# Performance work log

Measured on AMD Instinct MI355X. Metric: run time of the kernel, lower is better.

## Reference

```python
import jax, jax.numpy as jnp
import numpy as np

B, T, E, DK, H = 8, 2048, 1024, 64, 16  # dk*num_heads == embedding_dim


def setup_inputs() -> dict:
    key = jax.random.key(0)
    kx, kq, kk, kv, kl = jax.random.split(key, 5)
    x = jax.random.normal(kx, (B, T, E), dtype=jnp.float32)
    # zero-pad a random tail of each sequence so the data-derived padding mask
    # in the forward (length = count of nonzero energy[b,0,:]) is exercised
    lengths = jax.random.randint(kl, (B,), T // 2, T + 1)
    valid = (jnp.arange(T)[None, :, None] < lengths[:, None, None]).astype(jnp.float32)
    x = x * valid
    scale = 0.02
    Wq = jax.random.normal(kq, (E, DK * H), dtype=jnp.float32) * scale
    Wk = jax.random.normal(kk, (E, DK * H), dtype=jnp.float32) * scale
    Wv = jax.random.normal(kv, (E, DK * H), dtype=jnp.float32) * scale
    return {"x": x, "Wq": Wq, "Wk": Wk, "Wv": Wv}


def reference(x, Wq, Wk, Wv):
    # Q,K,V: [B, T, DK*H] (heads are fused, matching the source's bmm math)
    Q = jnp.einsum('bte,ed->btd', x, Wq)
    K = jnp.einsum('bte,ed->btd', x, Wk)
    V = jnp.einsum('bte,ed->btd', x, Wv)
    energy = jnp.einsum('btd,bsd->bts', Q, K)  # [B, T, T]
    # vectorized version of the per-batch loop: length from nonzeros of row 0,
    # then mask all key columns >= length with -inf
    lengths = jnp.sum(energy[:, 0, :] != 0, axis=-1)              # [B]
    col_mask = jnp.arange(T)[None, :] >= lengths[:, None]          # [B, T]
    energy = jnp.where(col_mask[:, None, :], -jnp.inf, energy)
    score = jax.nn.softmax(energy / jnp.sqrt(jnp.float32(DK)), axis=-1)
    return jnp.einsum('bts,bsd->btd', score, V)  # [B, T, DK*H]
```

## Files before the change

kernel.cpp:

```cpp
#include <hip/hip_runtime.h>
#include <hip/hip_bf16.h>


typedef unsigned short u16;
typedef __bf16 bf16x8 __attribute__((ext_vector_type(8)));
typedef float f32x4 __attribute__((ext_vector_type(4)));
typedef unsigned short us8 __attribute__((ext_vector_type(8)));

__device__ __forceinline__ u16 f2bf(float f) {
    union { float f; unsigned u; } x; x.f = f;
    unsigned r = x.u + 0x7FFFu + ((x.u >> 16) & 1u);
    return (u16)(r >> 16);
}
__device__ __forceinline__ u16 f2h(float f) {
    union { _Float16 h; u16 u; } c; c.h = (_Float16)f;
    return c.u;
}
__device__ __forceinline__ float h2f(u16 b) {
    union { u16 u; _Float16 h; } c; c.u = b;
    return (float)c.h;
}

__device__ __forceinline__ void gload_lds16(const void* g, void* l) {
    __builtin_amdgcn_global_load_lds(
        (const __attribute__((address_space(1))) unsigned*)g,
        (__attribute__((address_space(3))) unsigned*)l, 16, 0, 0);
}

__device__ __forceinline__ unsigned lds_off(const void* p) {
    return (unsigned)(size_t)(const __attribute__((address_space(3))) char*)p;
}
__device__ __forceinline__ bf16x8 ds_read16(unsigned a) {
    bf16x8 r;
    asm volatile("ds_read_b128 %0, %1" : "=v"(r) : "v"(a));
    return r;
}

__global__ void cast_x(const float* __restrict__ x, u16* __restrict__ o) {
    int i = blockIdx.x * 256 + threadIdx.x;
    float4 v = ((const float4*)x)[i];
    ushort4 u;
    u.x = f2bf(v.x); u.y = f2bf(v.y); u.z = f2bf(v.z); u.w = f2bf(v.w);
    ((ushort4*)o)[i] = u;
}

__global__ void transpose_cast_w(const float* __restrict__ Wq,
                                 const float* __restrict__ Wk,
                                 const float* __restrict__ Wv,
                                 u16* __restrict__ WT) {
    __shared__ float tile[32][33];
    const float* W = (blockIdx.z == 0) ? Wq : (blockIdx.z == 1) ? Wk : Wv;
    u16* T = WT + (size_t)blockIdx.z * 1048576;
    int n0 = blockIdx.x * 32, e0 = blockIdx.y * 32;
    int tx = threadIdx.x, ty = threadIdx.y;
#pragma unroll
    for (int j = 0; j < 4; ++j) {
        int e = ty + j * 8;
        tile[e][tx] = W[(size_t)(e0 + e) * 1024 + (n0 + tx)];
    }
    __syncthreads();
#pragma unroll
    for (int j = 0; j < 4; ++j) {
        int n = ty + j * 8;
        T[(size_t)(n0 + n) * 1024 + (e0 + tx)] = f2bf(tile[tx][n]);
    }
}

__global__ void calc_lengths(const float* __restrict__ x, int* __restrict__ len) {
    int b = blockIdx.x, tid = threadIdx.x;
    int cnt = 0;
    for (int t = tid; t < 2048; t += 256) {
        float4 v = *(const float4*)(x + ((size_t)b * 2048 + t) * 1024);
        cnt += (v.x != 0.f || v.y != 0.f || v.z != 0.f || v.w != 0.f) ? 1 : 0;
    }
#pragma unroll
    for (int off = 32; off; off >>= 1) cnt += __shfl_xor(cnt, off);
    __shared__ int red[4];
    int wid = tid >> 6, lane = tid & 63;
    if (!lane) red[wid] = cnt;
    __syncthreads();
    if (tid == 0) len[b] = red[0] + red[1] + red[2] + red[3];
}


#define SBAR0 __builtin_amdgcn_sched_barrier(0)

#define STAGE_T(KT, BUF) do { \
  _Pragma("unroll") for (int j_ = 0; j_ < 4; ++j_) \
      gload_lds16(A + offA[j_] + (size_t)(KT) * 64, &As[BUF][ldsC[j_]]); \
  _Pragma("unroll") for (int j_ = 0; j_ < 4; ++j_) \
      gload_lds16(B + offB[j_] + (size_t)(KT) * 64, &Bs[BUF][ldsC[j_]]); \
} while (0)

#define LD_A(S) do { \
  _Pragma("unroll") for (int mt_ = 0; mt_ < 4; ++mt_) \
    af[S][mt_] = ds_read16(rowA[mt_] + ((S) ? ps1 : ps0)); \
} while (0)
#define LD_B(S) do { \
  _Pragma("unroll") for (int nt_ = 0; nt_ < 4; ++nt_) \
    bf[S][nt_] = ds_read16(rowB[nt_] + ((S) ? ps1 : ps0)); \
} while (0)

#define MFMA_S(S) do { \
  _Pragma("unroll") for (int mt_ = 0; mt_ < 4; ++mt_) \
  _Pragma("unroll") for (int nt_ = 0; nt_ < 4; ++nt_) \
    acc[mt_][nt_] = __builtin_amdgcn_mfma_f32_16x16x32_bf16( \
        af[S][mt_], bf[S][nt_], acc[mt_][nt_], 0, 0, 0); \
} while (0)

template <int MODE>
__global__ __launch_bounds__(256, 2)
void gemm_bt(const u16* __restrict__ A, int lda, size_t sA,
             const u16* __restrict__ B, int ldb, size_t sB,
             void* __restrict__ Cv, void* __restrict__ Cv2,
             int ldc, size_t sC, int Kdim, const int* __restrict__ lenp) {
    __shared__ u16 As[2][128 * 64];
    __shared__ u16 Bs[2][128 * 64];
    const int tid = threadIdx.x;
    const int bz  = blockIdx.z;
    A += (size_t)bz * sA;
    B += (size_t)bz * sB;

    size_t bm, bn;
    if (MODE == 3) {
        int c    = blockIdx.x & 7;
        int s    = blockIdx.x >> 3;
        int half = (s >= 192) ? 1 : 0;
        int s2   = s - half * 192;
        int bx   = ((c + (half << 3)) << 3) + (s2 & 7);
        bm = (size_t)bx * 128;
        bn = (size_t)(s2 >> 3) * 128;
    } else {
        bm = (size_t)blockIdx.x * 128;
        bn = (size_t)blockIdx.y * 128;
    }

    bool skip = false;
    int kEnd = Kdim;
    if (MODE == 3) {
        int lenz = lenp[bm >> 11];
        skip = ((int)(bm & 2047) >= lenz);
    } else if (MODE == 4) {
        int lenz = lenp[bz];
        if ((int)bn >= lenz) return;
        skip = ((int)bm >= lenz);
    } else if (MODE == 5) {
        int lenz = lenp[bz];
        int r64 = (lenz + 63) & ~63;
        kEnd = r64 < Kdim ? r64 : Kdim;
    }

    const int wid = tid >> 6, lane = tid & 63;
    const int wm = wid >> 1, wn = wid & 1;
    const int q = lane >> 4, r = lane & 15;

    size_t offA[4], offB[4]; int ldsC[4];
#pragma unroll
    for (int j = 0; j < 4; ++j) {
        int c = j * 256 + tid;
        int row = c >> 3;
        int c16 = (c & 7) ^ (row & 7);
        offA[j] = (size_t)(bm + row) * lda + c16 * 8;
        offB[j] = (size_t)(bn + row) * ldb + c16 * 8;
        ldsC[j] = c * 8;
    }

    unsigned rowA[4], rowB[4], swz0, swz1;
    {
        unsigned asB = lds_off(&As[0][0]), bsB = lds_off(&Bs[0][0]);
        swz0 = (unsigned)((q ^ (r & 7)) * 16);
        swz1 = (unsigned)(((q + 4) ^ (r & 7)) * 16);
#pragma unroll
        for (int mt = 0; mt < 4; ++mt)
            rowA[mt] = asB + (unsigned)((wm * 64 + mt * 16 + r) * 128);
#pragma unroll
        for (int nt = 0; nt < 4; ++nt)
            rowB[nt] = bsB + (unsigned)((wn * 64 + nt * 16 + r) * 128);
    }

    f32x4 acc[4][4] = {};

    if (!skip) {
        const int NT = kEnd >> 6;
        STAGE_T(0, 0);
        STAGE_T(1, 1);
        asm volatile("s_waitcnt vmcnt(8)" ::: "memory");
        SBAR0; __builtin_amdgcn_s_barrier(); SBAR0;
        for (int t = 0; t < NT; ++t) {
            const int p = t & 1;
            const unsigned ps0 = (unsigned)(p << 14) + swz0;
            const unsigned ps1 = (unsigned)(p << 14) + swz1;
            bf16x8 af[2][4], bf[2][4];
            LD_A(0); LD_B(0);
            LD_A(1); LD_B(1);
            asm volatile("s_waitcnt lgkmcnt(8)" ::: "memory");
            SBAR0;
            __builtin_amdgcn_s_setprio(1);
            MFMA_S(0);
            __builtin_amdgcn_s_setprio(0);
            SBAR0;
            asm volatile("s_waitcnt lgkmcnt(0)" ::: "memory");
            SBAR0;
            __builtin_amdgcn_s_barrier();
            SBAR0;
            if (t + 2 < NT) STAGE_T(t + 2, p);
            SBAR0;
            __builtin_amdgcn_s_setprio(1);
            MFMA_S(1);
            __builtin_amdgcn_s_setprio(0);
            SBAR0;
            if (t + 2 < NT)      asm volatile("s_waitcnt vmcnt(8)" ::: "memory");
            else if (t + 1 < NT) asm volatile("s_waitcnt vmcnt(0)" ::: "memory");
            __builtin_amdgcn_s_barrier();
            SBAR0;
        }
    }

    if (MODE == 5) {
        float* C = (float*)Cv + (size_t)bz * sC;
#pragma unroll
        for (int mt = 0; mt < 4; ++mt) {
            size_t row = bm + wm * 64 + mt * 16 + q * 4;
#pragma unroll
            for (int nt = 0; nt < 4; ++nt) {
                size_t col = bn + wn * 64 + nt * 16 + r;
#pragma unroll
                for (int i = 0; i < 4; ++i)
                    C[(row + i) * (size_t)ldc + col] = acc[mt][nt][i];
            }
        }
    } else if (MODE == 4) {
        u16* C = (u16*)Cv + (size_t)bz * sC;
#pragma unroll
        for (int mt = 0; mt < 4; ++mt) {
            size_t row = bm + wm * 64 + mt * 16 + q * 4;
#pragma unroll
            for (int nt = 0; nt < 4; ++nt) {
                size_t col = bn + wn * 64 + nt * 16 + r;
#pragma unroll
                for (int i = 0; i < 4; ++i)
                    C[(row + i) * (size_t)ldc + col] = f2h(acc[mt][nt][i]);
            }
        }
    } else {
        int region = (int)(bn >> 10);
        if (region < 2) {
            u16* C = (u16*)Cv + (size_t)region * 16777216;
            size_t cb = bn - (size_t)region * 1024;
#pragma unroll
            for (int mt = 0; mt < 4; ++mt) {
                size_t row = bm + wm * 64 + mt * 16 + q * 4;
#pragma unroll
                for (int nt = 0; nt < 4; ++nt) {
                    size_t col = cb + wn * 64 + nt * 16 + r;
#pragma unroll
                    for (int i = 0; i < 4; ++i)
                        C[(row + i) * 1024 + col] = f2bf(acc[mt][nt][i]);
                }
            }
        } else {
            u16* Cb = (u16*)Cv2 + (bm >> 11) * (size_t)(1024 * 2048)
                      + (bn - 2048) * 2048 + (bm & 2047);
#pragma unroll
            for (int nt = 0; nt < 4; ++nt) {
                int cI = wn * 64 + nt * 16 + r;
#pragma unroll
                for (int mt = 0; mt < 4; ++mt) {
                    int tI = wm * 64 + mt * 16 + q * 4;
                    ushort4 o;
                    o.x = f2bf(acc[mt][nt][0]);
                    o.y = f2bf(acc[mt][nt][1]);
                    o.z = f2bf(acc[mt][nt][2]);
                    o.w = f2bf(acc[mt][nt][3]);
                    *(ushort4*)(Cb + (size_t)cI * 2048 + tI) = o;
                }
            }
        }
    }
}

__global__ void softmax_rows_w(u16* __restrict__ E, const int* __restrict__ lengths) {
    int row  = blockIdx.x * 4 + (threadIdx.x >> 6);
    int lane = threadIdx.x & 63;
    int len  = lengths[row >> 11];
    u16* e = E + (size_t)row * 2048;

    float vals[32];
#pragma unroll
    for (int j = 0; j < 4; ++j) {
        us8 v = ((const us8*)e)[j * 64 + lane];
#pragma unroll
        for (int w = 0; w < 8; ++w) vals[j * 8 + w] = h2f(v[w]);
    }

    float m = -3.4e38f;
#pragma unroll
    for (int j = 0; j < 4; ++j) {
        int base = (j * 64 + lane) * 8;
#pragma unroll
        for (int w = 0; w < 8; ++w)
            if (base + w < len) m = fmaxf(m, vals[j * 8 + w]);
    }
#pragma unroll
    for (int off = 32; off; off >>= 1) m = fmaxf(m, __shfl_xor(m, off));

    const float C = 0.18033688011112042f;
    float p[32]; float s = 0.f;
#pragma unroll
    for (int j = 0; j < 4; ++j) {
        int base = (j * 64 + lane) * 8;
#pragma unroll
        for (int w = 0; w < 8; ++w) {
            float v = (base + w < len) ? exp2f((vals[j * 8 + w] - m) * C) : 0.f;
            p[j * 8 + w] = v;
            s += v;
        }
    }
#pragma unroll
    for (int off = 32; off; off >>= 1) s += __shfl_xor(s, off);
    float rinv = 1.0f / s;

#pragma unroll
    for (int j = 0; j < 4; ++j) {
        us8 o;
#pragma unroll
        for (int w = 0; w < 8; ++w) o[w] = f2bf(p[j * 8 + w] * rinv);
        ((us8*)e)[j * 64 + lane] = o;
    }
}

extern "C" void kernel_launch(void* const* d_in, const int* in_sizes, int n_in,
                              void* d_out, int out_size, void* d_ws, size_t ws_size,
                              hipStream_t stream) {
    const float* x  = (const float*)d_in[0];
    const float* Wq = (const float*)d_in[1];
    const float* Wk = (const float*)d_in[2];
    const float* Wv = (const float*)d_in[3];
    float* out = (float*)d_out;
    char* ws = (char*)d_ws;

    const size_t SB  = 2097152;
    const size_t SBe = 4194304;

    if (ws_size < 140509440ULL) return;
    int* lengths = (int*)ws;
    u16* x16 = (u16*)(ws + 256);
    u16* WT  = (u16*)(ws + 33554688);
    u16* VT  = (u16*)(ws + 39846144);
    u16* E   = (u16*)(ws + 73400576);
    u16* Qb  = (u16*)d_out;
    u16* Kb  = Qb + 16777216;

    cast_x<<<dim3(16384), dim3(256), 0, stream>>>(x, x16);
    transpose_cast_w<<<dim3(32, 32, 3), dim3(32, 8), 0, stream>>>(Wq, Wk, Wv, WT);
    calc_lengths<<<dim3(8), dim3(256), 0, stream>>>(x, lengths);

    gemm_bt<3><<<dim3(3072, 1, 1), 256, 0, stream>>>(x16, 1024, 0, WT, 1024, 0,
                                                     Qb, VT, 1024, 0, 1024, lengths);

    gemm_bt<4><<<dim3(16, 16, 8), 256, 0, stream>>>(Qb, 1024, SB, Kb, 1024, SB,
                                                    E, nullptr, 2048, SBe, 1024, lengths);

    softmax_rows_w<<<dim3(4096), dim3(256), 0, stream>>>(E, lengths);

    gemm_bt<5><<<dim3(16, 8, 8), 256, 0, stream>>>(E, 2048, SBe, VT, 2048, SB,
                                                   out, nullptr, 1024, SB, 2048, lengths);
}
```

Baseline: 371.5 us.

## Fuse softmax into QK epilogue stats and PV GEMM operand exponentiation

Removes the standalone row-softmax pass over the score matrix. The QK^T GEMM epilogue now writes per-64-column partial max and sum-of-exponentials for each row. A small kernel reduces these into one log-sum-exp value per row. The PV GEMM applies exp2 with that offset to the A tiles after reading them from LDS and before the MFMAs. This saves a full read-modify-write of the large fp16 score buffer, but adds exp and conversion work inside the PV GEMM's inner loop and a shuffle reduction in the QK epilogue.

```diff
diff --git a/kernel.cpp b/kernel.cpp
--- a/kernel.cpp
+++ b/kernel.cpp
@@ -82,6 +82,21 @@
     if (tid == 0) len[b] = red[0] + red[1] + red[2] + red[3];
 }
 
+__global__ void reduce_stats(const float2* __restrict__ PM,
+                             float* __restrict__ st,
+                             const int* __restrict__ lengths) {
+    int row = blockIdx.x * 256 + threadIdx.x;
+    int len = lengths[row >> 11];
+    int nv = (len + 63) >> 6;
+    const float2* p = PM + (size_t)row * 32;
+    float m = -3.4e38f;
+    for (int j = 0; j < nv; ++j) m = fmaxf(m, p[j].x);
+    const float C = 0.18033688011112042f;
+    float l = 0.f;
+    for (int j = 0; j < nv; ++j) l += p[j].y * exp2f((p[j].x - m) * C);
+    st[row] = m * C + log2f(l);
+}
+
 
 #define SBAR0 __builtin_amdgcn_sched_barrier(0)
 
@@ -99,6 +114,18 @@
 #define LD_B(S) do { \
   _Pragma("unroll") for (int nt_ = 0; nt_ < 4; ++nt_) \
     bf[S][nt_] = ds_read16(rowB[nt_] + ((S) ? ps1 : ps0)); \
+} while (0)
+
+#define XF(S) do { \
+  _Pragma("unroll") for (int mt_ = 0; mt_ < 4; ++mt_) { \
+    us8 v_ = __builtin_bit_cast(us8, af[S][mt_]); \
+    us8 o_; \
+    _Pragma("unroll") for (int w_ = 0; w_ < 8; ++w_) { \
+      float e_ = h2f(v_[w_]); \
+      o_[w_] = f2bf(exp2f(e_ * 0.18033688011112042f - aS[mt_])); \
+    } \
+    af[S][mt_] = __builtin_bit_cast(bf16x8, o_); \
+  } \
 } while (0)
 
 #define MFMA_S(S) do { \
@@ -176,6 +203,14 @@
 #pragma unroll
         for (int nt = 0; nt < 4; ++nt)
             rowB[nt] = bsB + (unsigned)((wn * 64 + nt * 16 + r) * 128);
+    }
+
+    float aS[4] = {};
+    if (MODE == 5) {
+        const float* st = (const float*)Cv2;
+#pragma unroll
+        for (int mt = 0; mt < 4; ++mt)
+            aS[mt] = st[(size_t)bz * 2048 + bm + wm * 64 + mt * 16 + r];
     }
 
     f32x4 acc[4][4] = {};
@@ -195,12 +230,14 @@
             LD_A(1); LD_B(1);
             asm volatile("s_waitcnt lgkmcnt(8)" ::: "memory");
             SBAR0;
+            if (MODE == 5) XF(0);
             __builtin_amdgcn_s_setprio(1);
             MFMA_S(0);
             __builtin_amdgcn_s_setprio(0);
             SBAR0;
             asm volatile("s_waitcnt lgkmcnt(0)" ::: "memory");
             SBAR0;
+            if (MODE == 5) XF(1);
             __builtin_amdgcn_s_barrier();
             SBAR0;
             if (t + 2 < NT) STAGE_T(t + 2, p);
@@ -240,6 +277,43 @@
 #pragma unroll
                 for (int i = 0; i < 4; ++i)
                     C[(row + i) * (size_t)ldc + col] = f2h(acc[mt][nt][i]);
+            }
+        }
+        {
+            float2* PMp = (float2*)Cv2;
+            int lenz = lenp[bz];
+            int jcol = (int)(bn >> 6) + wn;
+            const float Cs = 0.18033688011112042f;
+#pragma unroll
+            for (int mt = 0; mt < 4; ++mt) {
+#pragma unroll
+                for (int i = 0; i < 4; ++i) {
+                    float vmax = -3.4e38f;
+#pragma unroll
+                    for (int nt = 0; nt < 4; ++nt) {
+                        int col = (int)bn + wn * 64 + nt * 16 + r;
+                        if (col < lenz)
+                            vmax = fmaxf(vmax, h2f(f2h(acc[mt][nt][i])));
+                    }
+#pragma unroll
+                    for (int off = 8; off; off >>= 1)
+                        vmax = fmaxf(vmax, __shfl_xor(vmax, off));
+                    float ssum = 0.f;
+#pragma unroll
+                    for (int nt = 0; nt < 4; ++nt) {
+                        int col = (int)bn + wn * 64 + nt * 16 + r;
+                        if (col < lenz)
+                            ssum += exp2f((h2f(f2h(acc[mt][nt][i])) - vmax) * Cs);
+                    }
+#pragma unroll
+                    for (int off = 8; off; off >>= 1)
+                        ssum += __shfl_xor(ssum, off);
+                    if (r == 0) {
+                        size_t row = (size_t)bz * 2048 + bm + wm * 64
+                                   + mt * 16 + q * 4 + i;
+                        PMp[row * 32 + jcol] = make_float2(vmax, ssum);
+                    }
+                }
             }
         }
     } else {
@@ -279,56 +353,6 @@
     }
 }
 
-__global__ void softmax_rows_w(u16* __restrict__ E, const int* __restrict__ lengths) {
-    int row  = blockIdx.x * 4 + (threadIdx.x >> 6);
-    int lane = threadIdx.x & 63;
-    int len  = lengths[row >> 11];
-    u16* e = E + (size_t)row * 2048;
-
-    float vals[32];
-#pragma unroll
-    for (int j = 0; j < 4; ++j) {
-        us8 v = ((const us8*)e)[j * 64 + lane];
-#pragma unroll
-        for (int w = 0; w < 8; ++w) vals[j * 8 + w] = h2f(v[w]);
-    }
-
-    float m = -3.4e38f;
-#pragma unroll
-    for (int j = 0; j < 4; ++j) {
-        int base = (j * 64 + lane) * 8;
-#pragma unroll
-        for (int w = 0; w < 8; ++w)
-            if (base + w < len) m = fmaxf(m, vals[j * 8 + w]);
-    }
-#pragma unroll
-    for (int off = 32; off; off >>= 1) m = fmaxf(m, __shfl_xor(m, off));
-
-    const float C = 0.18033688011112042f;
-    float p[32]; float s = 0.f;
-#pragma unroll
-    for (int j = 0; j < 4; ++j) {
-        int base = (j * 64 + lane) * 8;
-#pragma unroll
-        for (int w = 0; w < 8; ++w) {
-            float v = (base + w < len) ? exp2f((vals[j * 8 + w] - m) * C) : 0.f;
-            p[j * 8 + w] = v;
-            s += v;
-        }
-    }
-#pragma unroll
-    for (int off = 32; off; off >>= 1) s += __shfl_xor(s, off);
-    float rinv = 1.0f / s;
-
-#pragma unroll
-    for (int j = 0; j < 4; ++j) {
-        us8 o;
-#pragma unroll
-        for (int w = 0; w < 8; ++w) o[w] = f2bf(p[j * 8 + w] * rinv);
-        ((us8*)e)[j * 64 + lane] = o;
-    }
-}
-
 extern "C" void kernel_launch(void* const* d_in, const int* in_sizes, int n_in,
                               void* d_out, int out_size, void* d_ws, size_t ws_size,
                               hipStream_t stream) {
@@ -342,12 +366,14 @@
     const size_t SB  = 2097152;
     const size_t SBe = 4194304;
 
-    if (ws_size < 140509440ULL) return;
-    int* lengths = (int*)ws;
-    u16* x16 = (u16*)(ws + 256);
-    u16* WT  = (u16*)(ws + 33554688);
-    u16* VT  = (u16*)(ws + 39846144);
-    u16* E   = (u16*)(ws + 73400576);
+    if (ws_size < 144769280ULL) return;
+    int* lengths  = (int*)ws;
+    u16* x16      = (u16*)(ws + 256);
+    u16* WT       = (u16*)(ws + 33554688);
+    u16* VT       = (u16*)(ws + 39846144);
+    u16* E        = (u16*)(ws + 73400576);
+    float2* PM    = (float2*)(ws + 140509440);
+    float* stats  = (float*)(ws + 144703744);
     u16* Qb  = (u16*)d_out;
     u16* Kb  = Qb + 16777216;
 
@@ -359,10 +385,10 @@
                                                      Qb, VT, 1024, 0, 1024, lengths);
 
     gemm_bt<4><<<dim3(16, 16, 8), 256, 0, stream>>>(Qb, 1024, SB, Kb, 1024, SB,
-                                                    E, nullptr, 2048, SBe, 1024, lengths);
-
-    softmax_rows_w<<<dim3(4096), dim3(256), 0, stream>>>(E, lengths);
+                                                    E, PM, 2048, SBe, 1024, lengths);
+
+    reduce_stats<<<dim3(64), dim3(256), 0, stream>>>(PM, stats, lengths);
 
     gemm_bt<5><<<dim3(16, 8, 8), 256, 0, stream>>>(E, 2048, SBe, VT, 2048, SB,
-                                                   out, nullptr, 1024, SB, 2048, lengths);
-}
+                                                   out, stats, 1024, SB, 2048, lengths);
+}
```

After: 464.1 us. +24.9%, slower.
